# Kernel tuning notes

Hardware: AMD Instinct MI355X
Metric: run time of the kernel (lower is better)

## Reference

```python
import jax, jax.numpy as jnp
import numpy as np

B, L = 8, 512
D_MODEL, N_HEADS, N_LAYERS = 768, 12, 12
D_HEAD = D_MODEL // N_HEADS
D_FF = 4 * D_MODEL
NUM_LABELS = 1000
PATCH_DIM = 16 * 16 * 3
EPS = 1e-6


def setup_inputs() -> dict:
    key = jax.random.key(0)
    ks = jax.random.split(key, 24)
    d = D_MODEL

    def w(k, shape, fan_in):
        return (jax.random.normal(k, shape, jnp.float32) / np.sqrt(fan_in)).astype(jnp.float32)

    return {
        'patch': jax.random.normal(ks[0], (B, L, PATCH_DIM), jnp.float32),
        'box': jax.random.uniform(ks[1], (B, L, 4), jnp.float32),
        'patch_W': w(ks[2], (PATCH_DIM, d), PATCH_DIM),
        'patch_b': jnp.zeros((d,), jnp.float32),
        'box_W': w(ks[3], (d, d), d),
        'box_b': jnp.zeros((d,), jnp.float32),
        'Wq': w(ks[4], (N_LAYERS, d, d), d),
        'Wk': w(ks[5], (N_LAYERS, d, d), d),
        'Wv': w(ks[6], (N_LAYERS, d, d), d),
        'Wo': w(ks[7], (N_LAYERS, d, d), d),
        'attn_norm_w': jnp.ones((N_LAYERS, d), jnp.float32),
        'gate_W': w(ks[8], (N_LAYERS, d, D_FF), d),
        'hidden_W': w(ks[9], (N_LAYERS, d, D_FF), d),
        'ffn_out_W': w(ks[10], (N_LAYERS, D_FF, d), D_FF),
        'ffn_norm_w': jnp.ones((N_LAYERS, d), jnp.float32),
        'reward_norm_w': jnp.ones((d,), jnp.float32),
        'reward_W': w(ks[11], (d, 2), d),
        'reward_b': jnp.zeros((2,), jnp.float32),
        'label_norm_w': jnp.ones((d,), jnp.float32),
        'label_W': w(ks[12], (d, NUM_LABELS), d),
        'label_b': jnp.zeros((NUM_LABELS,), jnp.float32),
        'box_norm_w': jnp.ones((d,), jnp.float32),
        'boxh_W': w(ks[13], (d, 4), d),
        'boxh_b': jnp.zeros((4,), jnp.float32),
    }


def _rmsnorm(x, wgt):
    return x * jax.lax.rsqrt(jnp.mean(x * x, axis=-1, keepdims=True) + EPS) * wgt


def _rope(x, cos, sin):
    # x: [b, n, l, dh]; consecutive pairs form complex numbers (view_as_complex)
    xr, xi = x[..., 0::2], x[..., 1::2]
    out_r = xr * cos - xi * sin
    out_i = xr * sin + xi * cos
    return jnp.stack((out_r, out_i), axis=-1).reshape(x.shape)


def _forward(patch, box, patch_W, patch_b, box_W, box_b, Wq, Wk, Wv, Wo,
             attn_norm_w, gate_W, hidden_W, ffn_out_W, ffn_norm_w,
             reward_norm_w, reward_W, reward_b, label_norm_w, label_W, label_b,
             box_norm_w, boxh_W, boxh_b):
    b, l, _ = patch.shape
    d = D_MODEL
    # StackedSinusoidalEmbedding(d_model, 4): d_stack = d/4, theta over d_stack/2 freqs
    d_stack = d // 4
    theta_box = 1.0 / (10000.0 ** (2.0 * jnp.arange(d_stack // 2, dtype=jnp.float32) / d_stack))
    ang = box[..., None] * theta_box  # [b, l, 4, d_stack/2]
    box_sin = jnp.stack((jnp.cos(ang), jnp.sin(ang)), axis=-1).reshape(b, l, d)

    x = (patch @ patch_W + patch_b) + (box_sin @ box_W + box_b)

    # RoPE tables and causal mask (constants)
    theta = 1.0 / (10000.0 ** (2.0 * jnp.arange(D_HEAD // 2, dtype=jnp.float32) / D_HEAD))
    pos_ang = jnp.arange(l, dtype=jnp.float32)[:, None] * theta  # [l, dh/2]
    cos, sin = jnp.cos(pos_ang), jnp.sin(pos_ang)
    mask = jnp.triu(jnp.full((l, l), -jnp.inf, dtype=jnp.float32), 1)
    scale = jnp.float32(np.sqrt(D_HEAD))

    def block(h, p):
        wq, wk, wv, wo, anw, gw, hw, ow, fnw = p
        hn = _rmsnorm(h, anw)
        q = (hn @ wq).reshape(b, l, N_HEADS, D_HEAD).transpose(0, 2, 1, 3)
        k = (hn @ wk).reshape(b, l, N_HEADS, D_HEAD).transpose(0, 2, 1, 3)
        v = (hn @ wv).reshape(b, l, N_HEADS, D_HEAD).transpose(0, 2, 1, 3)
        scores = jnp.einsum('bnld,bnmd->bnlm', _rope(q, cos, sin), _rope(k, cos, sin)) / scale
        attn = jax.nn.softmax(scores + mask, axis=-1)
        o = jnp.einsum('bnlm,bnmd->bnld', attn, v).transpose(0, 2, 1, 3).reshape(b, l, d)
        h = h + o @ wo
        hn = _rmsnorm(h, fnw)
        h = h + (jax.nn.silu(hn @ gw) * (hn @ hw)) @ ow
        return h, None

    x, _ = jax.lax.scan(block, x, (Wq, Wk, Wv, Wo, attn_norm_w, gate_W, hidden_W, ffn_out_W, ffn_norm_w))

    reward = _rmsnorm(x, reward_norm_w) @ reward_W + reward_b
    label = _rmsnorm(x, label_norm_w) @ label_W + label_b
    box_out = _rmsnorm(x, box_norm_w) @ boxh_W + boxh_b
    return reward, label, box_out


def reference(patch, box, patch_W, patch_b, box_W, box_b, Wq, Wk, Wv, Wo,
              attn_norm_w, gate_W, hidden_W, ffn_out_W, ffn_norm_w,
              reward_norm_w, reward_W, reward_b, label_norm_w, label_W, label_b,
              box_norm_w, boxh_W, boxh_b):
    return _forward(patch, box, patch_W, patch_b, box_W, box_b, Wq, Wk, Wv, Wo,
                    attn_norm_w, gate_W, hidden_W, ffn_out_W, ffn_norm_w,
                    reward_norm_w, reward_W, reward_b, label_norm_w, label_W, label_b,
                    box_norm_w, boxh_W, boxh_b)
```

## Files before the change

kernel.cpp:

```cpp
#include <hip/hip_runtime.h>
#include <math.h>
#include <type_traits>

#define B_   8
#define L_   512
#define MTOK 4096
#define D_   768
#define NH_  12
#define DH_  64
#define DFF_ 3072
#define NL_  12

typedef unsigned short u16;
typedef __attribute__((ext_vector_type(4))) float f32x4;
typedef __attribute__((ext_vector_type(8))) short i16x8;
typedef __attribute__((ext_vector_type(8))) __bf16 b16x8;

template <typename A, typename = void>
struct PickFrag { using type = i16x8; };
template <typename A>
struct PickFrag<A, std::void_t<decltype(__builtin_amdgcn_mfma_f32_16x16x32_bf16(
    std::declval<A>(), std::declval<A>(), std::declval<f32x4>(), 0, 0, 0))>> {
  using type = A;
};
using frag_t = typename PickFrag<b16x8>::type;

#if __has_builtin(__builtin_amdgcn_global_load_lds)
#define HAS_GLDS 1
#else
#define HAS_GLDS 0
#endif

__device__ inline u16 f2bf(float f) {
    unsigned u = __float_as_uint(f);
    unsigned r = u + 0x7fffu + ((u >> 16) & 1u);
    return (u16)(r >> 16);
}
__device__ inline float bf2f(u16 b) { return __uint_as_float(((unsigned)b) << 16); }

__device__ inline void bar_raw() {
    asm volatile("" ::: "memory");
    __builtin_amdgcn_s_barrier();
    asm volatile("" ::: "memory");
}

__global__ void k_box_sin(u16* __restrict__ emb, const float* __restrict__ box) {
    int idx = blockIdx.x * blockDim.x + threadIdx.x;
    if (idx >= MTOK * D_) return;
    int t = idx / D_, d = idx % D_;
    int c = d / 192, r = d % 192, j = r >> 1;
    float theta = __expf(-(float)j * (9.210340371976184f / 96.0f));
    float ang = box[t * 4 + c] * theta;
    emb[(size_t)t * 1536 + 768 + d] = f2bf((r & 1) ? sinf(ang) : cosf(ang));
}

__global__ void k_cast(u16* __restrict__ emb, const float* __restrict__ in, int n4) {
    int i = blockIdx.x * blockDim.x + threadIdx.x;
    if (i >= n4) return;
    int t = i / 192, c4 = (i % 192) * 4;
    float4 v = *reinterpret_cast<const float4*>(in + (size_t)t * 768 + c4);
    unsigned lo = (unsigned)f2bf(v.x) | ((unsigned)f2bf(v.y) << 16);
    unsigned hi = (unsigned)f2bf(v.z) | ((unsigned)f2bf(v.w) << 16);
    *reinterpret_cast<uint2*>(emb + (size_t)t * 1536 + c4) = make_uint2(lo, hi);
}

__global__ void k_addb(float* __restrict__ dst, const float* __restrict__ a,
                       const float* __restrict__ b) {
    int i = blockIdx.x * blockDim.x + threadIdx.x;
    if (i < D_) dst[i] = a[i] + b[i];
}

__global__ __launch_bounds__(256) void k_convT(u16* __restrict__ dst,
                                               const float* __restrict__ src,
                                               int K, int N, int ld, int rs,
                                               int ro, int co) {
    __shared__ float t[32][33];
    int bn = blockIdx.x * 32;
    int bk = blockIdx.y * 32;
    int tx = threadIdx.x % 32, ty = threadIdx.x / 32;
    #pragma unroll
    for (int i = 0; i < 4; ++i) {
        int k = bk + ty + i * 8;
        int n = bn + tx;
        t[ty + i * 8][tx] = (n < N) ? src[(size_t)k * N + n] : 0.0f;
    }
    __syncthreads();
    #pragma unroll
    for (int i = 0; i < 4; ++i) {
        int n = bn + ty + i * 8;
        int k = bk + tx;
        dst[(size_t)(n * rs + ro) * ld + co + k] = f2bf(t[tx][ty + i * 8]);
    }
}


__global__ __launch_bounds__(256) void k_convT64(u16* __restrict__ dst,
                                                 const float* __restrict__ src,
                                                 int K, int N) {
    __shared__ float ts[32][65];
    const float* s = src + (size_t)blockIdx.z * K * N;
    u16* d = dst + (size_t)blockIdx.z * K * N;
    int bn = blockIdx.x * 32, bk = blockIdx.y * 64;
    int t = threadIdx.x, rn = t & 31;
    #pragma unroll
    for (int p = 0; p < 8; ++p) {
        int k = p * 8 + (t >> 5);
        ts[rn][k] = s[(size_t)(bk + k) * N + bn + rn];
    }
    __syncthreads();
    int n = t >> 3, kc = (t & 7) * 8;
    u16 tmp[8];
    #pragma unroll
    for (int j = 0; j < 8; ++j) tmp[j] = f2bf(ts[n][kc + j]);
    *reinterpret_cast<uint4*>(&d[(size_t)(bn + n) * K + bk + kc]) =
        *reinterpret_cast<uint4*>(tmp);
}

__global__ __launch_bounds__(256) void k_convT64_qkv(u16* __restrict__ dst,
                                                     const float* __restrict__ s0,
                                                     const float* __restrict__ s1,
                                                     const float* __restrict__ s2) {
    __shared__ float ts[32][65];
    int ly = blockIdx.z / 3, which = blockIdx.z % 3;
    const float* s = (which == 0 ? s0 : (which == 1 ? s1 : s2)) + (size_t)ly * 768 * 768;
    u16* d = dst + ((size_t)ly * 3 + which) * 768 * 768;
    int bn = blockIdx.x * 32, bk = blockIdx.y * 64;
    int t = threadIdx.x, rn = t & 31;
    #pragma unroll
    for (int p = 0; p < 8; ++p) {
        int k = p * 8 + (t >> 5);
        ts[rn][k] = s[(size_t)(bk + k) * 768 + bn + rn];
    }
    __syncthreads();
    int n = t >> 3, kc = (t & 7) * 8;
    u16 tmp[8];
    #pragma unroll
    for (int j = 0; j < 8; ++j) tmp[j] = f2bf(ts[n][kc + j]);
    *reinterpret_cast<uint4*>(&d[(size_t)(bn + n) * 768 + bk + kc]) =
        *reinterpret_cast<uint4*>(tmp);
}

__global__ __launch_bounds__(256) void k_convT64_gh(u16* __restrict__ dst,
                                                    const float* __restrict__ g,
                                                    const float* __restrict__ h) {
    __shared__ float ts[32][65];
    int ly = blockIdx.z >> 1, which = blockIdx.z & 1;
    const float* s = (which ? h : g) + (size_t)ly * 768 * 3072;
    u16* d = dst + (size_t)ly * 6144 * 768;
    int bn = blockIdx.x * 32, bk = blockIdx.y * 64;
    int t = threadIdx.x, rn = t & 31;
    #pragma unroll
    for (int p = 0; p < 8; ++p) {
        int k = p * 8 + (t >> 5);
        ts[rn][k] = s[(size_t)(bk + k) * 3072 + bn + rn];
    }
    __syncthreads();
    int n = t >> 3, kc = (t & 7) * 8;
    int ng = bn + n;
    int row = ((ng >> 4) << 5) + (ng & 15) + which * 16;
    u16 tmp[8];
    #pragma unroll
    for (int j = 0; j < 8; ++j) tmp[j] = f2bf(ts[n][kc + j]);
    *reinterpret_cast<uint4*>(&d[(size_t)row * 768 + bk + kc]) =
        *reinterpret_cast<uint4*>(tmp);
}

__global__ __launch_bounds__(256) void k_rmsnorm(u16* __restrict__ out,
                                                 const float* __restrict__ in,
                                                 const float* __restrict__ w) {
    int t = blockIdx.x;
    const float* x = in + (size_t)t * D_;
    float ss = 0.f;
    for (int i = threadIdx.x; i < D_; i += 256) { float v = x[i]; ss += v * v; }
    for (int off = 32; off > 0; off >>= 1) ss += __shfl_down(ss, off);
    __shared__ float red[4];
    int wid = threadIdx.x >> 6, lane = threadIdx.x & 63;
    if (lane == 0) red[wid] = ss;
    __syncthreads();
    float tot = red[0] + red[1] + red[2] + red[3];
    float inv = rsqrtf(tot / (float)D_ + 1e-6f);
    for (int i = threadIdx.x; i < D_; i += 256)
        out[(size_t)t * D_ + i] = f2bf(x[i] * inv * w[i]);
}

template <int S>
__global__ __launch_bounds__(256) void k_fused_rr(float* __restrict__ h,
                                                  const float* __restrict__ part,
                                                  u16* __restrict__ hn,
                                                  const float* __restrict__ w) {
    int t = blockIdx.x;
    size_t base = (size_t)t * D_;
    float x[3];
    float ss = 0.f;
    #pragma unroll
    for (int c = 0; c < 3; ++c) {
        int i = threadIdx.x + c * 256;
        float v = h[base + i];
        #pragma unroll
        for (int s = 0; s < S; ++s)
            v += part[(size_t)s * MTOK * D_ + base + i];
        x[c] = v;
        h[base + i] = v;
        ss += v * v;
    }
    for (int off = 32; off > 0; off >>= 1) ss += __shfl_down(ss, off);
    __shared__ float red[4];
    int wid = threadIdx.x >> 6, lane = threadIdx.x & 63;
    if (lane == 0) red[wid] = ss;
    __syncthreads();
    float tot = red[0] + red[1] + red[2] + red[3];
    float inv = rsqrtf(tot / (float)D_ + 1e-6f);
    #pragma unroll
    for (int c = 0; c < 3; ++c) {
        int i = threadIdx.x + c * 256;
        hn[base + i] = f2bf(x[c] * inv * w[i]);
    }
}

__global__ void k_rope_tab(float* __restrict__ tab) {
    int idx = blockIdx.x * blockDim.x + threadIdx.x;
    if (idx >= L_ * 32) return;
    int l = idx >> 5, j = idx & 31;
    float theta = __expf(-(float)j * (9.210340371976184f / 32.0f));
    float s, c;
    sincosf((float)l * theta, &s, &c);
    tab[idx * 2] = c;
    tab[idx * 2 + 1] = s;
}

template <int MODE>
__global__ __launch_bounds__(256) void k_gemm_bf16(void* __restrict__ Cp,
                                                   const u16* __restrict__ A,
                                                   const u16* __restrict__ BT,
                                                   const float* __restrict__ bias,
                                                   int K, int Nout, int ldC) {
    __shared__ u16 smem[16384];
    int tid = threadIdx.x;
    int wid = tid >> 6, lane = tid & 63;

    int nx = gridDim.x, ny = gridDim.y, nz = gridDim.z;
    int bid = ((blockIdx.z * ny) + blockIdx.y) * nx + blockIdx.x;
    int nwg = nx * ny * nz;
    int cpx = nwg >> 3;
    int swz = (bid & 7) * cpx + (bid >> 3);
    int sk  = swz / (nx * ny);
    int rem = swz % (nx * ny);
    int by = rem / nx, bx = rem % nx;
    int row0 = by * 128, col0 = bx * 128;
    int wr = wid >> 1, wc = wid & 1;

    int Klen = K / nz;
    int kbeg = sk * Klen;

    int c0 = wid * 128 + lane;
    int c1 = c0 + 64;
    int r0 = c0 >> 2, kc0 = (c0 & 3) * 8;
    int r1 = c1 >> 2, kc1 = (c1 & 3) * 8;
    const u16* gA0 = A  + (size_t)(row0 + r0) * K + kbeg + kc0;
    const u16* gA1 = A  + (size_t)(row0 + r1) * K + kbeg + kc1;
    const u16* gB0 = BT + (size_t)(col0 + r0) * K + kbeg + kc0;
    const u16* gB1 = BT + (size_t)(col0 + r1) * K + kbeg + kc1;

    auto stage = [&](int buf, int kt) {
        u16* Asb = smem + buf * 4096;
        u16* Bsb = smem + 8192 + buf * 4096;
#if HAS_GLDS
        __builtin_amdgcn_global_load_lds(
            (const __attribute__((address_space(1))) void*)(gA0 + kt),
            (__attribute__((address_space(3))) void*)&Asb[c0 * 8], 16, 0, 0);
        __builtin_amdgcn_global_load_lds(
            (const __attribute__((address_space(1))) void*)(gA1 + kt),
            (__attribute__((address_space(3))) void*)&Asb[c1 * 8], 16, 0, 0);
        __builtin_amdgcn_global_load_lds(
            (const __attribute__((address_space(1))) void*)(gB0 + kt),
            (__attribute__((address_space(3))) void*)&Bsb[c0 * 8], 16, 0, 0);
        __builtin_amdgcn_global_load_lds(
            (const __attribute__((address_space(1))) void*)(gB1 + kt),
            (__attribute__((address_space(3))) void*)&Bsb[c1 * 8], 16, 0, 0);
#else
        *reinterpret_cast<uint4*>(&Asb[c0 * 8]) = *reinterpret_cast<const uint4*>(gA0 + kt);
        *reinterpret_cast<uint4*>(&Asb[c1 * 8]) = *reinterpret_cast<const uint4*>(gA1 + kt);
        *reinterpret_cast<uint4*>(&Bsb[c0 * 8]) = *reinterpret_cast<const uint4*>(gB0 + kt);
        *reinterpret_cast<uint4*>(&Bsb[c1 * 8]) = *reinterpret_cast<const uint4*>(gB1 + kt);
#endif
    };

    f32x4 acc[4][4] = {};
    int lrow = lane & 15, lk = (lane >> 4) * 8;

    stage(0, 0);
    int cur = 0;
    for (int kt = 0; kt < Klen; kt += 32) {
        bool has_next = (kt + 32 < Klen);
        if (has_next) stage(cur ^ 1, kt + 32);
        if (has_next) asm volatile("s_waitcnt vmcnt(4) lgkmcnt(0)" ::: "memory");
        else          asm volatile("s_waitcnt vmcnt(0) lgkmcnt(0)" ::: "memory");
        __builtin_amdgcn_sched_barrier(0);
        bar_raw();
        const u16* Asb = smem + cur * 4096;
        const u16* Bsb = smem + 8192 + cur * 4096;
        frag_t af[4], bfr[4];
        #pragma unroll
        for (int m = 0; m < 4; ++m)
            af[m] = *reinterpret_cast<const frag_t*>(&Asb[(wr * 64 + m * 16 + lrow) * 32 + lk]);
        #pragma unroll
        for (int n = 0; n < 4; ++n)
            bfr[n] = *reinterpret_cast<const frag_t*>(&Bsb[(wc * 64 + n * 16 + lrow) * 32 + lk]);
        #pragma unroll
        for (int m = 0; m < 4; ++m)
            #pragma unroll
            for (int n = 0; n < 4; ++n)
                acc[m][n] = __builtin_amdgcn_mfma_f32_16x16x32_bf16(af[m], bfr[n], acc[m][n], 0, 0, 0);
        bar_raw();
        cur ^= 1;
    }

    int lcol = lane & 15, rb = (lane >> 4) * 4;

    if (MODE == 6) {
        u16* qkvh = (u16*)Cp;
        const float* tab = bias;
        if (col0 >= 1536) {
            int head_base = (col0 - 1536) >> 6;
            int bb = row0 >> 9;
            int l0 = row0 & 511;
            #pragma unroll
            for (int pass = 0; pass < 2; ++pass) {
                if (wc == pass) {
                    #pragma unroll
                    for (int m = 0; m < 4; ++m) {
                        #pragma unroll
                        for (int n = 0; n < 4; ++n) {
                            int dl = n * 16 + lcol;
                            int rl = wr * 64 + m * 16 + rb;
                            u16 tmp[4];
                            #pragma unroll
                            for (int e = 0; e < 4; ++e) tmp[e] = f2bf(acc[m][n][e]);
                            *reinterpret_cast<uint2*>(&smem[dl * 136 + rl]) =
                                *reinterpret_cast<uint2*>(tmp);
                        }
                    }
                }
                __syncthreads();
                int head = head_base + pass;
                size_t vbase = (size_t)2 * MTOK * 768 +
                               ((size_t)(bb * NH_ + head) * 64) * 512;
                #pragma unroll
                for (int it = 0; it < 4; ++it) {
                    int dd = it * 16 + (tid >> 4);
                    int rr = (tid & 15) * 8;
                    uint4 v4 = *reinterpret_cast<const uint4*>(&smem[dd * 136 + rr]);
                    *reinterpret_cast<uint4*>(&qkvh[vbase + (size_t)dd * 512 + l0 + rr]) = v4;
                }
                __syncthreads();
            }
        } else {
            int sec = col0 / 768;
            float qscale = (sec == 0) ? 0.125f : 1.0f;
            #pragma unroll
            for (int m = 0; m < 4; ++m) {
                #pragma unroll
                for (int n = 0; n < 4; ++n) {
                    int col = col0 + wc * 64 + n * 16 + lcol;
                    int head = (col % 768) >> 6;
                    int d = col & 63;
                    #pragma unroll
                    for (int e = 0; e < 4; ++e) {
                        int row = row0 + wr * 64 + m * 16 + rb + e;
                        int bb = row >> 9, l = row & 511;
                        float v = acc[m][n][e];
                        float p = __shfl_xor(v, 1);
                        float2 cs = *reinterpret_cast<const float2*>(
                            tab + ((size_t)l * 32 + (d >> 1)) * 2);
                        float r = (d & 1) ? (p * cs.y + v * cs.x)
                                          : (v * cs.x - p * cs.y);
                        r *= qscale;
                        qkvh[(size_t)sec * MTOK * 768 +
                             ((size_t)(bb * NH_ + head) * 512 + l) * 64 + d] = f2bf(r);
                    }
                }
            }
        }
        return;
    }

    if (MODE == 5) {
        #pragma unroll
        for (int m = 0; m < 4; ++m) {
            #pragma unroll
            for (int np = 0; np < 2; ++np) {
                int ocol = (col0 >> 1) + wc * 32 + np * 16 + lcol;
                #pragma unroll
                for (int e = 0; e < 4; ++e) {
                    int row = row0 + wr * 64 + m * 16 + rb + e;
                    float g = acc[m][2 * np][e], hv = acc[m][2 * np + 1][e];
                    float s = g / (1.0f + __expf(-g));
                    ((u16*)Cp)[(size_t)row * ldC + ocol] = f2bf(s * hv);
                }
            }
        }
        return;
    }

    float* Cpart = (MODE == 4)
        ? ((float*)Cp + (size_t)sk * (size_t)(ny * 128) * ldC) : (float*)Cp;
    #pragma unroll
    for (int m = 0; m < 4; ++m) {
        #pragma unroll
        for (int n = 0; n < 4; ++n) {
            int col = col0 + wc * 64 + n * 16 + lcol;
            if (col >= Nout) continue;
            #pragma unroll
            for (int e = 0; e < 4; ++e) {
                int row = row0 + wr * 64 + m * 16 + rb + e;
                float v = acc[m][n][e];
                size_t off = (size_t)row * ldC + col;
                if (MODE == 0) {
                    if (bias) v += bias[col];
                    ((float*)Cp)[off] = v;
                } else if (MODE == 3) {
                    ((u16*)Cp)[off] = f2bf(v);
                } else if (MODE == 4) {
                    Cpart[off] = v;
                }
            }
        }
    }
}

__global__ __launch_bounds__(256) void k_attn3(u16* __restrict__ o,
                                               const u16* __restrict__ qh,
                                               const u16* __restrict__ kh,
                                               const u16* __restrict__ vT) {
    int bh = blockIdx.x, qb = blockIdx.y;
    int b = bh / NH_, hh = bh % NH_;
    int tid = threadIdx.x, wid = tid >> 6, lane = tid & 63;
    __shared__ u16 Qs[64][72], Ks[64][72], Vs[64][72], Ps[64][72];

    #pragma unroll
    for (int i = 0; i < 2; ++i) {
        int idx = tid + i * 256;
        int r = idx >> 3, c8 = (idx & 7) * 8;
        uint4 v4 = *reinterpret_cast<const uint4*>(
            qh + ((size_t)bh * L_ + qb * 64 + r) * 64 + c8);
        *reinterpret_cast<uint4*>(&Qs[r][c8]) = v4;
    }
    __syncthreads();

    int lr = lane & 15, lg = lane >> 4;
    frag_t aq[2];
    #pragma unroll
    for (int kd = 0; kd < 2; ++kd)
        aq[kd] = *reinterpret_cast<const frag_t*>(&Qs[wid * 16 + lr][kd * 32 + lg * 8]);

    f32x4 accO[4] = {};
    float M[4], S[4];
    #pragma unroll
    for (int e = 0; e < 4; ++e) { M[e] = -INFINITY; S[e] = 0.f; }

    for (int kb = 0; kb <= qb; ++kb) {
        __syncthreads();
        #pragma unroll
        for (int i = 0; i < 2; ++i) {
            int idx = tid + i * 256;
            int r = idx >> 3, c8 = (idx & 7) * 8;
            *reinterpret_cast<uint4*>(&Ks[r][c8]) = *reinterpret_cast<const uint4*>(
                kh + ((size_t)bh * L_ + kb * 64 + r) * 64 + c8);
            *reinterpret_cast<uint4*>(&Vs[r][c8]) = *reinterpret_cast<const uint4*>(
                vT + ((size_t)bh * 64 + r) * L_ + kb * 64 + c8);
        }
        __syncthreads();

        f32x4 sv[4];
        __builtin_amdgcn_s_setprio(1);
        #pragma unroll
        for (int ct = 0; ct < 4; ++ct) {
            frag_t bk0 = *reinterpret_cast<const frag_t*>(&Ks[ct * 16 + lr][lg * 8]);
            frag_t bk1 = *reinterpret_cast<const frag_t*>(&Ks[ct * 16 + lr][32 + lg * 8]);
            f32x4 z = {0.f, 0.f, 0.f, 0.f};
            z = __builtin_amdgcn_mfma_f32_16x16x32_bf16(aq[0], bk0, z, 0, 0, 0);
            sv[ct] = __builtin_amdgcn_mfma_f32_16x16x32_bf16(aq[1], bk1, z, 0, 0, 0);
        }
        __builtin_amdgcn_s_setprio(0);

        bool diag = (kb == qb);
        float esc[4];
        #pragma unroll
        for (int e = 0; e < 4; ++e) {
            int qg = qb * 64 + wid * 16 + lg * 4 + e;
            float mx = -1e30f;
            #pragma unroll
            for (int ct = 0; ct < 4; ++ct) {
                float s = sv[ct][e];
                if (diag && (kb * 64 + ct * 16 + lr > qg)) s = -1e30f;
                sv[ct][e] = s;
                mx = fmaxf(mx, s);
            }
            #pragma unroll
            for (int msk = 8; msk; msk >>= 1) mx = fmaxf(mx, __shfl_xor(mx, msk));
            float newM = fmaxf(M[e], mx);
            float ps = 0.f;
            #pragma unroll
            for (int ct = 0; ct < 4; ++ct) {
                float p = __expf(sv[ct][e] - newM);
                sv[ct][e] = p;
                ps += p;
            }
            #pragma unroll
            for (int msk = 8; msk; msk >>= 1) ps += __shfl_xor(ps, msk);
            esc[e] = __expf(M[e] - newM);
            S[e] = S[e] * esc[e] + ps;
            M[e] = newM;
        }
        #pragma unroll
        for (int dt = 0; dt < 4; ++dt)
            #pragma unroll
            for (int e = 0; e < 4; ++e) accO[dt][e] *= esc[e];

        #pragma unroll
        for (int ct = 0; ct < 4; ++ct)
            #pragma unroll
            for (int e = 0; e < 4; ++e)
                Ps[wid * 16 + lg * 4 + e][ct * 16 + lr] = f2bf(sv[ct][e]);

        frag_t pa0 = *reinterpret_cast<const frag_t*>(&Ps[wid * 16 + lr][lg * 8]);
        frag_t pa1 = *reinterpret_cast<const frag_t*>(&Ps[wid * 16 + lr][32 + lg * 8]);
        __builtin_amdgcn_s_setprio(1);
        #pragma unroll
        for (int dt = 0; dt < 4; ++dt) {
            frag_t bv0 = *reinterpret_cast<const frag_t*>(&Vs[dt * 16 + lr][lg * 8]);
            frag_t bv1 = *reinterpret_cast<const frag_t*>(&Vs[dt * 16 + lr][32 + lg * 8]);
            accO[dt] = __builtin_amdgcn_mfma_f32_16x16x32_bf16(pa0, bv0, accO[dt], 0, 0, 0);
            accO[dt] = __builtin_amdgcn_mfma_f32_16x16x32_bf16(pa1, bv1, accO[dt], 0, 0, 0);
        }
        __builtin_amdgcn_s_setprio(0);
    }

    #pragma unroll
    for (int dt = 0; dt < 4; ++dt) {
        #pragma unroll
        for (int e = 0; e < 4; ++e) {
            int row = b * L_ + qb * 64 + wid * 16 + lg * 4 + e;
            o[(size_t)row * D_ + hh * 64 + dt * 16 + lr] = f2bf(accO[dt][e] / S[e]);
        }
    }
}

__global__ __launch_bounds__(256) void k_heads3(float* __restrict__ out_reward,
                                                float* __restrict__ out_box,
                                                const float* __restrict__ h,
                                                const float* __restrict__ rnw,
                                                const float* __restrict__ rW,
                                                const float* __restrict__ rb,
                                                const float* __restrict__ bnw,
                                                const float* __restrict__ bW,
                                                const float* __restrict__ bb) {
    int t = blockIdx.x;
    size_t base = (size_t)t * D_;
    float x[3];
    float ss = 0.f;
    #pragma unroll
    for (int c = 0; c < 3; ++c) {
        int i = threadIdx.x + c * 256;
        x[c] = h[base + i];
        ss += x[c] * x[c];
    }
    for (int off = 32; off > 0; off >>= 1) ss += __shfl_down(ss, off);
    __shared__ float red[4];
    int wid = threadIdx.x >> 6, lane = threadIdx.x & 63;
    if (lane == 0) red[wid] = ss;
    __syncthreads();
    float inv = rsqrtf((red[0] + red[1] + red[2] + red[3]) / (float)D_ + 1e-6f);

    float a[6] = {};
    #pragma unroll
    for (int c = 0; c < 3; ++c) {
        int i = threadIdx.x + c * 256;
        float xr = x[c] * inv;
        float xw = xr * rnw[i];
        a[0] += xw * rW[i * 2];
        a[1] += xw * rW[i * 2 + 1];
        float xb = xr * bnw[i];
        #pragma unroll
        for (int j = 0; j < 4; ++j) a[2 + j] += xb * bW[i * 4 + j];
    }
    #pragma unroll
    for (int j = 0; j < 6; ++j)
        for (int off = 32; off > 0; off >>= 1) a[j] += __shfl_down(a[j], off);
    __shared__ float red2[4][6];
    if (lane == 0)
        #pragma unroll
        for (int j = 0; j < 6; ++j) red2[wid][j] = a[j];
    __syncthreads();
    if (threadIdx.x < 6) {
        float s = red2[0][threadIdx.x] + red2[1][threadIdx.x] +
                  red2[2][threadIdx.x] + red2[3][threadIdx.x];
        if (threadIdx.x < 2) out_reward[(size_t)t * 2 + threadIdx.x] = s + rb[threadIdx.x];
        else                 out_box[(size_t)t * 4 + threadIdx.x - 2] = s + bb[threadIdx.x - 2];
    }
}

extern "C" void kernel_launch(void* const* d_in, const int* in_sizes, int n_in,
                              void* d_out, int out_size, void* d_ws, size_t ws_size,
                              hipStream_t stream) {
    const float* patch        = (const float*)d_in[0];
    const float* box          = (const float*)d_in[1];
    const float* patch_W      = (const float*)d_in[2];
    const float* patch_b      = (const float*)d_in[3];
    const float* box_W        = (const float*)d_in[4];
    const float* box_b        = (const float*)d_in[5];
    const float* Wq           = (const float*)d_in[6];
    const float* Wk           = (const float*)d_in[7];
    const float* Wv           = (const float*)d_in[8];
    const float* Wo           = (const float*)d_in[9];
    const float* attn_norm_w  = (const float*)d_in[10];
    const float* gate_W       = (const float*)d_in[11];
    const float* hidden_W     = (const float*)d_in[12];
    const float* ffn_out_W    = (const float*)d_in[13];
    const float* ffn_norm_w   = (const float*)d_in[14];
    const float* reward_norm_w= (const float*)d_in[15];
    const float* reward_W     = (const float*)d_in[16];
    const float* reward_b     = (const float*)d_in[17];
    const float* label_norm_w = (const float*)d_in[18];
    const float* label_W      = (const float*)d_in[19];
    const float* label_b      = (const float*)d_in[20];
    const float* box_norm_w   = (const float*)d_in[21];
    const float* boxh_W       = (const float*)d_in[22];
    const float* boxh_b       = (const float*)d_in[23];

    char* w = (char*)d_ws;
    auto alloc = [&](size_t bytes) { char* p = w; w += (bytes + 255) & ~(size_t)255; return p; };

    u16*  wqkv_a = (u16*)alloc((size_t)NL_ * 2304 * 768 * 2);
    u16*  wo_a   = (u16*)alloc((size_t)NL_ * 768 * 768 * 2);
    u16*  wgh_a  = (u16*)alloc((size_t)NL_ * 6144 * 768 * 2);
    u16*  wfo_a  = (u16*)alloc((size_t)NL_ * 768 * 3072 * 2);
    u16*  wcat   = (u16*)alloc((size_t)768 * 1536 * 2);
    u16*  wlab   = (u16*)alloc((size_t)1024 * 768 * 2);
    float* bias_c= (float*)alloc((size_t)768 * 4);
    u16*  emb    = (u16*)alloc((size_t)MTOK * 1536 * 2);
    float* h     = (float*)alloc((size_t)MTOK * D_ * 4);
    u16*  hn_bf  = (u16*)alloc((size_t)MTOK * D_ * 2);
    u16*  qkvh   = (u16*)alloc((size_t)MTOK * 2304 * 2);
    float* tab   = (float*)alloc((size_t)L_ * 32 * 2 * 4);
    u16*  o_bf   = (u16*)alloc((size_t)MTOK * D_ * 2);
    u16*  ga_bf  = (u16*)alloc((size_t)MTOK * DFF_ * 2);
    float* part  = (float*)alloc((size_t)4 * MTOK * D_ * 4);

    u16* qh = qkvh;
    u16* kh = qkvh + (size_t)MTOK * 768;
    u16* vT = qkvh + (size_t)2 * MTOK * 768;

    dim3 blk(256);

    k_convT<<<dim3(24, 24), blk, 0, stream>>>(wcat, patch_W, 768, 768, 1536, 1, 0, 0);
    k_convT<<<dim3(24, 24), blk, 0, stream>>>(wcat, box_W,   768, 768, 1536, 1, 0, 768);
    k_convT<<<dim3(32, 24), blk, 0, stream>>>(wlab, label_W, 768, 1000, 768, 1, 0, 0);
    k_addb<<<3, blk, 0, stream>>>(bias_c, patch_b, box_b);
    k_rope_tab<<<(L_ * 32 + 255) / 256, blk, 0, stream>>>(tab);
    k_convT64_qkv<<<dim3(24, 12, 36), blk, 0, stream>>>(wqkv_a, Wq, Wk, Wv);
    k_convT64<<<dim3(24, 12, 12), blk, 0, stream>>>(wo_a, Wo, 768, 768);
    k_convT64_gh<<<dim3(96, 12, 24), blk, 0, stream>>>(wgh_a, gate_W, hidden_W);
    k_convT64<<<dim3(24, 48, 12), blk, 0, stream>>>(wfo_a, ffn_out_W, 3072, 768);
    k_cast<<<(MTOK * 768 / 4 + 255) / 256, blk, 0, stream>>>(emb, patch, MTOK * 768 / 4);
    k_box_sin<<<(MTOK * D_ + 255) / 256, blk, 0, stream>>>(emb, box);

    k_gemm_bf16<0><<<dim3(6, 32), blk, 0, stream>>>(h, emb, wcat, bias_c, 1536, 768, 768);
    k_rmsnorm<<<MTOK, blk, 0, stream>>>(hn_bf, h, attn_norm_w);

    for (int ly = 0; ly < NL_; ++ly) {
        const u16* wqkv = wqkv_a + (size_t)ly * 2304 * 768;
        const u16* wo_l = wo_a   + (size_t)ly * 768 * 768;
        const u16* wgh  = wgh_a  + (size_t)ly * 6144 * 768;
        const u16* wfo  = wfo_a  + (size_t)ly * 768 * 3072;
        const float* fnw = ffn_norm_w + (size_t)ly * D_;
        const float* nxt = (ly + 1 < NL_) ? attn_norm_w + (size_t)(ly + 1) * D_
                                          : label_norm_w;

        k_gemm_bf16<6><<<dim3(18, 32), blk, 0, stream>>>(qkvh, hn_bf, wqkv, tab, 768, 2304, 2304);
        k_attn3<<<dim3(96, 8), blk, 0, stream>>>(o_bf, qh, kh, vT);
        k_gemm_bf16<4><<<dim3(6, 32, 2), blk, 0, stream>>>(part, o_bf, wo_l, nullptr, 768, 768, 768);
        k_fused_rr<2><<<MTOK, blk, 0, stream>>>(h, part, hn_bf, fnw);

        k_gemm_bf16<5><<<dim3(48, 32), blk, 0, stream>>>(ga_bf, hn_bf, wgh, nullptr, 768, 6144, 3072);
        k_gemm_bf16<4><<<dim3(6, 32, 4), blk, 0, stream>>>(part, ga_bf, wfo, nullptr, 3072, 768, 768);
        k_fused_rr<4><<<MTOK, blk, 0, stream>>>(h, part, hn_bf, nxt);
    }

    float* out_reward = (float*)d_out;
    float* out_label  = out_reward + (size_t)MTOK * 2;
    float* out_box    = out_label + (size_t)MTOK * 1000;

    k_gemm_bf16<0><<<dim3(8, 32), blk, 0, stream>>>(out_label, hn_bf, wlab, label_b, 768, 1000, 1000);
    k_heads3<<<MTOK, blk, 0, stream>>>(out_reward, out_box, h,
                                       reward_norm_w, reward_W, reward_b,
                                       box_norm_w, boxh_W, boxh_b);
}
```

Before: 2.317 ms.

## Prefetch K/V tiles into registers with swizzled LDS; widen weight-transpose tiles

```diff
diff --git a/kernel.cpp b/kernel.cpp
--- a/kernel.cpp
+++ b/kernel.cpp
@@ -44,6 +44,8 @@
     asm volatile("" ::: "memory");
 }
 
+__device__ inline int swz8(int row, int c8) { return c8 ^ ((row & 7) << 3); }
+
 __global__ void k_box_sin(u16* __restrict__ emb, const float* __restrict__ box) {
     int idx = blockIdx.x * blockDim.x + threadIdx.x;
     if (idx >= MTOK * D_) return;
@@ -94,75 +96,78 @@
 }
 
 
-__global__ __launch_bounds__(256) void k_convT64(u16* __restrict__ dst,
-                                                 const float* __restrict__ src,
-                                                 int K, int N) {
-    __shared__ float ts[32][65];
+__global__ __launch_bounds__(256) void k_convT128(u16* __restrict__ dst,
+                                                  const float* __restrict__ src,
+                                                  int K, int N) {
+    __shared__ float ts[32][130];
     const float* s = src + (size_t)blockIdx.z * K * N;
     u16* d = dst + (size_t)blockIdx.z * K * N;
-    int bn = blockIdx.x * 32, bk = blockIdx.y * 64;
-    int t = threadIdx.x, rn = t & 31;
-    #pragma unroll
-    for (int p = 0; p < 8; ++p) {
-        int k = p * 8 + (t >> 5);
+    int bn = blockIdx.x * 32, bk = blockIdx.y * 128;
+    int t = threadIdx.x, rn = t & 31, kr = t >> 5;
+    #pragma unroll
+    for (int p = 0; p < 16; ++p) {
+        int k = p * 8 + kr;
         ts[rn][k] = s[(size_t)(bk + k) * N + bn + rn];
     }
     __syncthreads();
-    int n = t >> 3, kc = (t & 7) * 8;
-    u16 tmp[8];
-    #pragma unroll
-    for (int j = 0; j < 8; ++j) tmp[j] = f2bf(ts[n][kc + j]);
-    *reinterpret_cast<uint4*>(&d[(size_t)(bn + n) * K + bk + kc]) =
-        *reinterpret_cast<uint4*>(tmp);
-}
-
-__global__ __launch_bounds__(256) void k_convT64_qkv(u16* __restrict__ dst,
-                                                     const float* __restrict__ s0,
-                                                     const float* __restrict__ s1,
-                                                     const float* __restrict__ s2) {
-    __shared__ float ts[32][65];
+    int n = t >> 3, kc = (t & 7) * 16;
+    u16 tmp[16];
+    #pragma unroll
+    for (int j = 0; j < 16; ++j) tmp[j] = f2bf(ts[n][kc + j]);
+    u16* dp = &d[(size_t)(bn + n) * K + bk + kc];
+    *reinterpret_cast<uint4*>(dp)     = *reinterpret_cast<uint4*>(tmp);
+    *reinterpret_cast<uint4*>(dp + 8) = *reinterpret_cast<uint4*>(tmp + 8);
+}
+
+__global__ __launch_bounds__(256) void k_convT128_qkv(u16* __restrict__ dst,
+                                                      const float* __restrict__ s0,
+                                                      const float* __restrict__ s1,
+                                                      const float* __restrict__ s2) {
+    __shared__ float ts[32][130];
     int ly = blockIdx.z / 3, which = blockIdx.z % 3;
     const float* s = (which == 0 ? s0 : (which == 1 ? s1 : s2)) + (size_t)ly * 768 * 768;
     u16* d = dst + ((size_t)ly * 3 + which) * 768 * 768;
-    int bn = blockIdx.x * 32, bk = blockIdx.y * 64;
-    int t = threadIdx.x, rn = t & 31;
-    #pragma unroll
-    for (int p = 0; p < 8; ++p) {
-        int k = p * 8 + (t >> 5);
+    int bn = blockIdx.x * 32, bk = blockIdx.y * 128;
+    int t = threadIdx.x, rn = t & 31, kr = t >> 5;
+    #pragma unroll
+    for (int p = 0; p < 16; ++p) {
+        int k = p * 8 + kr;
         ts[rn][k] = s[(size_t)(bk + k) * 768 + bn + rn];
     }
     __syncthreads();
-    int n = t >> 3, kc = (t & 7) * 8;
-    u16 tmp[8];
-    #pragma unroll
-    for (int j = 0; j < 8; ++j) tmp[j] = f2bf(ts[n][kc + j]);
-    *reinterpret_cast<uint4*>(&d[(size_t)(bn + n) * 768 + bk + kc]) =
-        *reinterpret_cast<uint4*>(tmp);
-}
-
-__global__ __launch_bounds__(256) void k_convT64_gh(u16* __restrict__ dst,
-                                                    const float* __restrict__ g,
-                                                    const float* __restrict__ h) {
-    __shared__ float ts[32][65];
+    int n = t >> 3, kc = (t & 7) * 16;
+    u16 tmp[16];
+    #pragma unroll
+    for (int j = 0; j < 16; ++j) tmp[j] = f2bf(ts[n][kc + j]);
+    u16* dp = &d[(size_t)(bn + n) * 768 + bk + kc];
+    *reinterpret_cast<uint4*>(dp)     = *reinterpret_cast<uint4*>(tmp);
+    *reinterpret_cast<uint4*>(dp + 8) = *reinterpret_cast<uint4*>(tmp + 8);
+}
+
+__global__ __launch_bounds__(256) void k_convT128_gh(u16* __restrict__ dst,
+                                                     const float* __restrict__ g,
+                                                     const float* __restrict__ h) {
+    __shared__ float ts[32][130];
     int ly = blockIdx.z >> 1, which = blockIdx.z & 1;
     const float* s = (which ? h : g) + (size_t)ly * 768 * 3072;
     u16* d = dst + (size_t)ly * 6144 * 768;
-    int bn = blockIdx.x * 32, bk = blockIdx.y * 64;
-    int t = threadIdx.x, rn = t & 31;
-    #pragma unroll
-    for (int p = 0; p < 8; ++p) {
-        int k = p * 8 + (t >> 5);
+    int bn = blockIdx.x * 32, bk = blockIdx.y * 128;
+    int t = threadIdx.x, rn = t & 31, kr = t >> 5;
+    #pragma unroll
+    for (int p = 0; p < 16; ++p) {
+        int k = p * 8 + kr;
         ts[rn][k] = s[(size_t)(bk + k) * 3072 + bn + rn];
     }
     __syncthreads();
-    int n = t >> 3, kc = (t & 7) * 8;
+    int n = t >> 3, kc = (t & 7) * 16;
     int ng = bn + n;
     int row = ((ng >> 4) << 5) + (ng & 15) + which * 16;
-    u16 tmp[8];
-    #pragma unroll
-    for (int j = 0; j < 8; ++j) tmp[j] = f2bf(ts[n][kc + j]);
-    *reinterpret_cast<uint4*>(&d[(size_t)row * 768 + bk + kc]) =
-        *reinterpret_cast<uint4*>(tmp);
+    u16 tmp[16];
+    #pragma unroll
+    for (int j = 0; j < 16; ++j) tmp[j] = f2bf(ts[n][kc + j]);
+    u16* dp = &d[(size_t)row * 768 + bk + kc];
+    *reinterpret_cast<uint4*>(dp)     = *reinterpret_cast<uint4*>(tmp);
+    *reinterpret_cast<uint4*>(dp + 8) = *reinterpret_cast<uint4*>(tmp + 8);
 }
 
 __global__ __launch_bounds__(256) void k_rmsnorm(u16* __restrict__ out,
@@ -435,7 +440,8 @@
     int bh = blockIdx.x, qb = blockIdx.y;
     int b = bh / NH_, hh = bh % NH_;
     int tid = threadIdx.x, wid = tid >> 6, lane = tid & 63;
-    __shared__ u16 Qs[64][72], Ks[64][72], Vs[64][72], Ps[64][72];
+    __shared__ u16 Qs[64][72], Ps[64][72];
+    __shared__ u16 Ks[64 * 64], Vs[64 * 64];
 
     #pragma unroll
     for (int i = 0; i < 2; ++i) {
@@ -453,30 +459,41 @@
     for (int kd = 0; kd < 2; ++kd)
         aq[kd] = *reinterpret_cast<const frag_t*>(&Qs[wid * 16 + lr][kd * 32 + lg * 8]);
 
+    int sr0 = tid >> 3, sc8 = (tid & 7) * 8;
+    int sr1 = sr0 + 32;
+
     f32x4 accO[4] = {};
     float M[4], S[4];
     #pragma unroll
     for (int e = 0; e < 4; ++e) { M[e] = -INFINITY; S[e] = 0.f; }
 
+    uint4 kreg0 = *reinterpret_cast<const uint4*>(kh + ((size_t)bh * L_ + sr0) * 64 + sc8);
+    uint4 kreg1 = *reinterpret_cast<const uint4*>(kh + ((size_t)bh * L_ + sr1) * 64 + sc8);
+    uint4 vreg0 = *reinterpret_cast<const uint4*>(vT + ((size_t)bh * 64 + sr0) * L_ + sc8);
+    uint4 vreg1 = *reinterpret_cast<const uint4*>(vT + ((size_t)bh * 64 + sr1) * L_ + sc8);
+
     for (int kb = 0; kb <= qb; ++kb) {
         __syncthreads();
-        #pragma unroll
-        for (int i = 0; i < 2; ++i) {
-            int idx = tid + i * 256;
-            int r = idx >> 3, c8 = (idx & 7) * 8;
-            *reinterpret_cast<uint4*>(&Ks[r][c8]) = *reinterpret_cast<const uint4*>(
-                kh + ((size_t)bh * L_ + kb * 64 + r) * 64 + c8);
-            *reinterpret_cast<uint4*>(&Vs[r][c8]) = *reinterpret_cast<const uint4*>(
-                vT + ((size_t)bh * 64 + r) * L_ + kb * 64 + c8);
+        *reinterpret_cast<uint4*>(&Ks[sr0 * 64 + swz8(sr0, sc8)]) = kreg0;
+        *reinterpret_cast<uint4*>(&Ks[sr1 * 64 + swz8(sr1, sc8)]) = kreg1;
+        *reinterpret_cast<uint4*>(&Vs[sr0 * 64 + swz8(sr0, sc8)]) = vreg0;
+        *reinterpret_cast<uint4*>(&Vs[sr1 * 64 + swz8(sr1, sc8)]) = vreg1;
+        __syncthreads();
+        if (kb < qb) {
+            int nb = (kb + 1) * 64;
+            kreg0 = *reinterpret_cast<const uint4*>(kh + ((size_t)bh * L_ + nb + sr0) * 64 + sc8);
+            kreg1 = *reinterpret_cast<const uint4*>(kh + ((size_t)bh * L_ + nb + sr1) * 64 + sc8);
+            vreg0 = *reinterpret_cast<const uint4*>(vT + ((size_t)bh * 64 + sr0) * L_ + nb + sc8);
+            vreg1 = *reinterpret_cast<const uint4*>(vT + ((size_t)bh * 64 + sr1) * L_ + nb + sc8);
         }
-        __syncthreads();
 
         f32x4 sv[4];
         __builtin_amdgcn_s_setprio(1);
         #pragma unroll
         for (int ct = 0; ct < 4; ++ct) {
-            frag_t bk0 = *reinterpret_cast<const frag_t*>(&Ks[ct * 16 + lr][lg * 8]);
-            frag_t bk1 = *reinterpret_cast<const frag_t*>(&Ks[ct * 16 + lr][32 + lg * 8]);
+            int krow = ct * 16 + lr;
+            frag_t bk0 = *reinterpret_cast<const frag_t*>(&Ks[krow * 64 + swz8(krow, lg * 8)]);
+            frag_t bk1 = *reinterpret_cast<const frag_t*>(&Ks[krow * 64 + swz8(krow, 32 + lg * 8)]);
             f32x4 z = {0.f, 0.f, 0.f, 0.f};
             z = __builtin_amdgcn_mfma_f32_16x16x32_bf16(aq[0], bk0, z, 0, 0, 0);
             sv[ct] = __builtin_amdgcn_mfma_f32_16x16x32_bf16(aq[1], bk1, z, 0, 0, 0);
@@ -528,8 +545,9 @@
         __builtin_amdgcn_s_setprio(1);
         #pragma unroll
         for (int dt = 0; dt < 4; ++dt) {
-            frag_t bv0 = *reinterpret_cast<const frag_t*>(&Vs[dt * 16 + lr][lg * 8]);
-            frag_t bv1 = *reinterpret_cast<const frag_t*>(&Vs[dt * 16 + lr][32 + lg * 8]);
+            int vrow = dt * 16 + lr;
+            frag_t bv0 = *reinterpret_cast<const frag_t*>(&Vs[vrow * 64 + swz8(vrow, lg * 8)]);
+            frag_t bv1 = *reinterpret_cast<const frag_t*>(&Vs[vrow * 64 + swz8(vrow, 32 + lg * 8)]);
             accO[dt] = __builtin_amdgcn_mfma_f32_16x16x32_bf16(pa0, bv0, accO[dt], 0, 0, 0);
             accO[dt] = __builtin_amdgcn_mfma_f32_16x16x32_bf16(pa1, bv1, accO[dt], 0, 0, 0);
         }
@@ -658,10 +676,10 @@
     k_convT<<<dim3(32, 24), blk, 0, stream>>>(wlab, label_W, 768, 1000, 768, 1, 0, 0);
     k_addb<<<3, blk, 0, stream>>>(bias_c, patch_b, box_b);
     k_rope_tab<<<(L_ * 32 + 255) / 256, blk, 0, stream>>>(tab);
-    k_convT64_qkv<<<dim3(24, 12, 36), blk, 0, stream>>>(wqkv_a, Wq, Wk, Wv);
-    k_convT64<<<dim3(24, 12, 12), blk, 0, stream>>>(wo_a, Wo, 768, 768);
-    k_convT64_gh<<<dim3(96, 12, 24), blk, 0, stream>>>(wgh_a, gate_W, hidden_W);
-    k_convT64<<<dim3(24, 48, 12), blk, 0, stream>>>(wfo_a, ffn_out_W, 3072, 768);
+    k_convT128_qkv<<<dim3(24, 6, 36), blk, 0, stream>>>(wqkv_a, Wq, Wk, Wv);
+    k_convT128<<<dim3(24, 6, 12), blk, 0, stream>>>(wo_a, Wo, 768, 768);
+    k_convT128_gh<<<dim3(96, 6, 24), blk, 0, stream>>>(wgh_a, gate_W, hidden_W);
+    k_convT128<<<dim3(24, 24, 12), blk, 0, stream>>>(wfo_a, ffn_out_W, 3072, 768);
     k_cast<<<(MTOK * 768 / 4 + 255) / 256, blk, 0, stream>>>(emb, patch, MTOK * 768 / 4);
     k_box_sin<<<(MTOK * D_ + 255) / 256, blk, 0, stream>>>(emb, box);
 
```

Measured after the change: 2.319 ms. Within noise of the previous version (+0.1%).
